# Optimization experiments

Hardware: AMD Instinct MI355X
Metric: run time of the kernel (lower is better)

## Reference

```python
import jax, jax.numpy as jnp
import numpy as np

B, IN, H = 4096, 1024, 2048


def setup_inputs() -> dict:
    key = jax.random.key(0)
    ks = jax.random.split(key, 7)
    return {
        "x": jax.random.normal(ks[0], (B, IN), jnp.float32),
        "h": jax.random.normal(ks[1], (B, H), jnp.float32),
        "c": jax.random.normal(ks[2], (B, H), jnp.float32),
        "w_ih": jax.random.normal(ks[3], (4 * H, IN), jnp.float32) * 0.02,
        "w_hh": jax.random.normal(ks[4], (4 * H, H), jnp.float32) * 0.02,
        "b_ih": jax.random.normal(ks[5], (4 * H,), jnp.float32) * 0.02,
        "b_hh": jax.random.normal(ks[6], (4 * H,), jnp.float32) * 0.02,
    }


def reference(x, h, c, w_ih, w_hh, b_ih, b_hh):
    act = jnp.sin  # custom gate activation (Sine_activation repo)
    # Combined GEMMs: same math as the 8 separate F.linear calls.
    # gates: [B, 4H], chunk order along dim 0 of weights: f, i, ic, o
    gates = (x @ w_ih.T + b_ih) + (h @ w_hh.T + b_hh)
    f_in, i_in, ic_in, o_in = jnp.split(gates, 4, axis=-1)
    ft = jax.nn.sigmoid(f_in)
    it = jax.nn.sigmoid(i_in)
    i_cands = act(ic_in)
    ct = c * ft + i_cands * it
    ot = jax.nn.sigmoid(o_in)
    ht = ot * act(ct)
    return (ht, ct)
```

## Files before the change

### kernel.cpp

```cpp
#include <hip/hip_runtime.h>

typedef __attribute__((ext_vector_type(8))) short short8;
typedef __attribute__((ext_vector_type(4))) float f32x4;

#define BDIM 4096
#define INDIM 1024
#define HDIM 2048
#define KDIM 3072
#define NDIM 8192
#define OUT_HALF 8388608
#define NKT 96

__device__ __forceinline__ unsigned short f2bf(float f) {
  unsigned u = __float_as_uint(f);
  u += 0x7FFFu + ((u >> 16) & 1u);
  return (unsigned short)(u >> 16);
}

__device__ __forceinline__ float sigmoidf_(float x) {
  return 1.0f / (1.0f + __expf(-x));
}

__global__ __launch_bounds__(256) void pack_a(const float* __restrict__ x,
                                              const float* __restrict__ hh,
                                              unsigned short* __restrict__ A) {
  int idx = blockIdx.x * 256 + threadIdx.x;
  int m = idx / 384;
  int k0 = (idx - m * 384) * 8;
  const float* src = (k0 < INDIM) ? (x + (size_t)m * INDIM + k0)
                                  : (hh + (size_t)m * HDIM + (k0 - INDIM));
  float4 lo = ((const float4*)src)[0];
  float4 hi = ((const float4*)src)[1];
  union { unsigned short us[8]; uint4 v; } o;
  o.us[0] = f2bf(lo.x); o.us[1] = f2bf(lo.y); o.us[2] = f2bf(lo.z); o.us[3] = f2bf(lo.w);
  o.us[4] = f2bf(hi.x); o.us[5] = f2bf(hi.y); o.us[6] = f2bf(hi.z); o.us[7] = f2bf(hi.w);
  *(uint4*)(A + (size_t)m * KDIM + k0) = o.v;
}

__global__ __launch_bounds__(256) void pack_w(const float* __restrict__ w_ih,
                                              const float* __restrict__ w_hh,
                                              const float* __restrict__ b_ih,
                                              const float* __restrict__ b_hh,
                                              unsigned short* __restrict__ W,
                                              float* __restrict__ bias) {
  int idx = blockIdx.x * 256 + threadIdx.x;
  int np = idx / 384;
  int rem = idx - np * 384;
  int k0 = rem * 8;
  int j = np >> 2;
  int g = np & 3;
  int n = g * HDIM + j;
  const float* src = (k0 < INDIM) ? (w_ih + (size_t)n * INDIM + k0)
                                  : (w_hh + (size_t)n * HDIM + (k0 - INDIM));
  float4 lo = ((const float4*)src)[0];
  float4 hi = ((const float4*)src)[1];
  union { unsigned short us[8]; uint4 v; } o;
  o.us[0] = f2bf(lo.x); o.us[1] = f2bf(lo.y); o.us[2] = f2bf(lo.z); o.us[3] = f2bf(lo.w);
  o.us[4] = f2bf(hi.x); o.us[5] = f2bf(hi.y); o.us[6] = f2bf(hi.z); o.us[7] = f2bf(hi.w);
  *(uint4*)(W + (size_t)np * KDIM + k0) = o.v;
  if (rem == 0) bias[np] = b_ih[n] + b_hh[n];
}

__device__ __forceinline__ void gload_lds16(const void* g, void* l) {
  __builtin_amdgcn_global_load_lds(
      (const __attribute__((address_space(1))) void*)g,
      (__attribute__((address_space(3))) void*)l, 16, 0, 0);
}

#define SB0 __builtin_amdgcn_sched_barrier(0)

__global__ __launch_bounds__(512, 2) void lstm_gemm(
    const unsigned short* __restrict__ A,
    const unsigned short* __restrict__ W,
    const float* __restrict__ bias,
    const float* __restrict__ c,
    float* __restrict__ out) {
  extern __shared__ char smem[];

  const int tid = threadIdx.x;
  const int lane = tid & 63;
  const int wid = tid >> 6;

  const int bid = blockIdx.x;
  const int local = bid >> 3;
  const int tm = (bid & 7) * 2 + (local & 1);
  const int tn = local >> 1;

  int rowA0, clA0, rowA1, clA1;
  {
    int P0 = wid * 1024 + lane * 16;
    int P1 = 8192 + wid * 1024 + lane * 16;
    int r2, cp, cg;
    r2 = P0 >> 7; cp = (P0 >> 4) & 7; cg = cp ^ (r2 & 7);
    rowA0 = r2 * 2 + (cg >> 2); clA0 = cg & 3;
    r2 = P1 >> 7; cp = (P1 >> 4) & 7; cg = cp ^ (r2 & 7);
    rowA1 = r2 * 2 + (cg >> 2); clA1 = cg & 3;
  }
  const unsigned short* srcA0 = A + (size_t)(tm * 256 + rowA0) * KDIM + clA0 * 8;
  const unsigned short* srcA1 = A + (size_t)(tm * 256 + rowA1) * KDIM + clA1 * 8;
  const unsigned short* srcB0 = W + (size_t)(tn * 256 + rowA0) * KDIM + clA0 * 8;
  const unsigned short* srcB1 = W + (size_t)(tn * 256 + rowA1) * KDIM + clA1 * 8;
  const int ldA0 = wid * 1024;
  const int ldA1 = 8192 + wid * 1024;
  const int ldB0 = 16384 + wid * 1024;
  const int ldB1 = 24576 + wid * 1024;

  const int fr = lane & 15;
  const int fq = lane >> 4;
  const int wr = wid >> 2;
  const int wc = wid & 3;
  const int frh = fr >> 1;
  const int clA = (((fr & 1) << 2) | fq) ^ frh;
  const int aconst = wr * 8192 + frh * 128 + clA * 16;
  const int bconst = 16384 + wc * 4096 + frh * 128 + clA * 16;

  f32x4 acc[8][4] = {};
  short8 af[4], bf_[4], ag[4];

#pragma unroll
  for (int tt = 0; tt < 3; ++tt) {
    char* lb = smem + tt * 32768;
    gload_lds16(srcA0 + tt * 32, lb + ldA0);
    gload_lds16(srcA1 + tt * 32, lb + ldA1);
    gload_lds16(srcB0 + tt * 32, lb + ldB0);
    gload_lds16(srcB1 + tt * 32, lb + ldB1);
  }
  asm volatile("s_waitcnt vmcnt(8)" ::: "memory");
  __builtin_amdgcn_s_barrier(); SB0;
#pragma unroll
  for (int mi = 0; mi < 4; ++mi)
    af[mi] = *(const short8*)(smem + aconst + mi * 1024);
#pragma unroll
  for (int ni = 0; ni < 4; ++ni)
    bf_[ni] = *(const short8*)(smem + bconst + ni * 1024);

#define TILE_BODY(T, VMSTR, STAGE_, PREF_)                                   \
  do {                                                                       \
    const char* rb = smem + ((T) & 3) * 32768;                               \
    const char* rbn = smem + (((T) + 1) & 3) * 32768;                        \
    char* lb = smem + (((T) + 3) & 3) * 32768;                               \
    if (STAGE_) {                                                            \
      gload_lds16(srcA0 + (size_t)((T) + 3) * 32, lb + ldA0);                \
      gload_lds16(srcA1 + (size_t)((T) + 3) * 32, lb + ldA1);                \
    }                                                                        \
    _Pragma("unroll")                                                        \
    for (int mi = 0; mi < 4; ++mi)                                           \
      ag[mi] = *(const short8*)(rb + aconst + (mi + 4) * 1024);              \
    SB0;                                                                     \
    __builtin_amdgcn_s_setprio(1);                                           \
    _Pragma("unroll")                                                        \
    for (int mi = 0; mi < 4; ++mi)                                           \
      _Pragma("unroll")                                                      \
      for (int ni = 0; ni < 4; ++ni)                                         \
        acc[mi][ni] = __builtin_amdgcn_mfma_f32_16x16x32_bf16(               \
            af[mi], bf_[ni], acc[mi][ni], 0, 0, 0);                          \
    __builtin_amdgcn_s_setprio(0);                                           \
    if (STAGE_) {                                                            \
      gload_lds16(srcB0 + (size_t)((T) + 3) * 32, lb + ldB0);                \
      gload_lds16(srcB1 + (size_t)((T) + 3) * 32, lb + ldB1);                \
    }                                                                        \
    asm volatile("s_waitcnt vmcnt(" VMSTR ")" ::: "memory");                 \
    asm volatile("s_waitcnt lgkmcnt(0)" ::: "memory");                       \
    __builtin_amdgcn_s_barrier(); SB0;                                       \
    if (PREF_) {                                                             \
      _Pragma("unroll")                                                      \
      for (int mi = 0; mi < 4; ++mi)                                         \
        af[mi] = *(const short8*)(rbn + aconst + mi * 1024);                 \
    }                                                                        \
    SB0;                                                                     \
    __builtin_amdgcn_s_setprio(1);                                           \
    _Pragma("unroll")                                                        \
    for (int mi = 0; mi < 4; ++mi)                                           \
      _Pragma("unroll")                                                      \
      for (int ni = 0; ni < 4; ++ni)                                         \
        acc[mi + 4][ni] = __builtin_amdgcn_mfma_f32_16x16x32_bf16(           \
            ag[mi], bf_[ni], acc[mi + 4][ni], 0, 0, 0);                      \
    __builtin_amdgcn_s_setprio(0);                                           \
    if (PREF_) {                                                             \
      _Pragma("unroll")                                                      \
      for (int ni = 0; ni < 4; ++ni)                                         \
        bf_[ni] = *(const short8*)(rbn + bconst + ni * 1024);                \
    }                                                                        \
  } while (0)

  for (int t = 0; t < NKT - 3; ++t) TILE_BODY(t, "8", true, true);
  TILE_BODY(NKT - 3, "4", false, true);
  TILE_BODY(NKT - 2, "0", false, true);
  TILE_BODY(NKT - 1, "0", false, false);
#undef TILE_BODY

  const int jw = fr;
  const int jg = tn * 64 + wc * 16 + jw;
  const f32x4 bi = *(const f32x4*)(bias + tn * 256 + wc * 64 + jw * 4);
  float* ep = (float*)smem + wid * 1024;

#pragma unroll
  for (int mi = 0; mi < 8; ++mi) {
#pragma unroll
    for (int ni = 0; ni < 4; ++ni)
#pragma unroll
      for (int r = 0; r < 4; ++r)
        ep[(fq * 4 + r) * 64 + ni * 16 + fr] = acc[mi][ni][r];
    asm volatile("s_waitcnt lgkmcnt(0)" ::: "memory");
#pragma unroll
    for (int t4 = 0; t4 < 4; ++t4) {
      const int row = fq + t4 * 4;
      f32x4 g4 = *(const f32x4*)(ep + row * 64 + jw * 4);
      const float f_in = g4[0] + bi[0];
      const float i_in = g4[1] + bi[1];
      const float ic_in = g4[2] + bi[2];
      const float o_in = g4[3] + bi[3];
      const float ft = sigmoidf_(f_in);
      const float it = sigmoidf_(i_in);
      const float ics = __sinf(ic_in);
      const int mg = tm * 256 + wr * 128 + mi * 16 + row;
      const float cv = c[(size_t)mg * HDIM + jg];
      const float ct = cv * ft + ics * it;
      const float ot = sigmoidf_(o_in);
      const float ht = ot * __sinf(ct);
      out[(size_t)mg * HDIM + jg] = ht;
      out[OUT_HALF + (size_t)mg * HDIM + jg] = ct;
    }
    asm volatile("s_waitcnt lgkmcnt(0)" ::: "memory");
  }
}

extern "C" void kernel_launch(void* const* d_in, const int* in_sizes, int n_in,
                              void* d_out, int out_size, void* d_ws, size_t ws_size,
                              hipStream_t stream) {
  const float* x    = (const float*)d_in[0];
  const float* h    = (const float*)d_in[1];
  const float* c    = (const float*)d_in[2];
  const float* w_ih = (const float*)d_in[3];
  const float* w_hh = (const float*)d_in[4];
  const float* b_ih = (const float*)d_in[5];
  const float* b_hh = (const float*)d_in[6];
  float* out = (float*)d_out;

  char* ws = (char*)d_ws;
  unsigned short* Abf = (unsigned short*)ws;
  unsigned short* Wbf = (unsigned short*)(ws + 25165824);
  float* bias = (float*)(ws + 25165824 + 50331648);

  hipFuncSetAttribute((const void*)lstm_gemm,
                      hipFuncAttributeMaxDynamicSharedMemorySize, 131072);

  pack_a<<<6144, 256, 0, stream>>>(x, h, Abf);
  pack_w<<<12288, 256, 0, stream>>>(w_ih, w_hh, b_ih, b_hh, Wbf, bias);
  lstm_gemm<<<512, 512, 131072, stream>>>(Abf, Wbf, bias, c, out);
}
```

Before: 222.6 us.

## Shrink GEMM block tile to 128x256 with 4 waves and triple-buffered LDS

New measurement: 258.3 us. 1.16x slower.

```diff
diff --git a/kernel.cpp b/kernel.cpp
--- a/kernel.cpp
+++ b/kernel.cpp
@@ -10,6 +10,7 @@
 #define NDIM 8192
 #define OUT_HALF 8388608
 #define NKT 96
+#define BUFB 24576
 
 __device__ __forceinline__ unsigned short f2bf(float f) {
   unsigned u = __float_as_uint(f);
@@ -69,7 +70,7 @@
 
 #define SB0 __builtin_amdgcn_sched_barrier(0)
 
-__global__ __launch_bounds__(512, 2) void lstm_gemm(
+__global__ __launch_bounds__(256, 2) void lstm_gemm(
     const unsigned short* __restrict__ A,
     const unsigned short* __restrict__ W,
     const float* __restrict__ bias,
@@ -83,69 +84,74 @@
 
   const int bid = blockIdx.x;
   const int local = bid >> 3;
-  const int tm = (bid & 7) * 2 + (local & 1);
-  const int tn = local >> 1;
-
-  int rowA0, clA0, rowA1, clA1;
-  {
-    int P0 = wid * 1024 + lane * 16;
-    int P1 = 8192 + wid * 1024 + lane * 16;
-    int r2, cp, cg;
-    r2 = P0 >> 7; cp = (P0 >> 4) & 7; cg = cp ^ (r2 & 7);
-    rowA0 = r2 * 2 + (cg >> 2); clA0 = cg & 3;
-    r2 = P1 >> 7; cp = (P1 >> 4) & 7; cg = cp ^ (r2 & 7);
-    rowA1 = r2 * 2 + (cg >> 2); clA1 = cg & 3;
+  const int tn = (bid & 7) * 4 + (local >> 5);
+  const int tm = local & 31;
+
+  int rowQ[4], colQ[4];
+#pragma unroll
+  for (int q = 0; q < 4; ++q) {
+    int P = q * 4096 + wid * 1024 + lane * 16;
+    int r2 = P >> 7, cp = (P >> 4) & 7, cg = cp ^ (r2 & 7);
+    rowQ[q] = r2 * 2 + (cg >> 2);
+    colQ[q] = (cg & 3) * 8;
   }
-  const unsigned short* srcA0 = A + (size_t)(tm * 256 + rowA0) * KDIM + clA0 * 8;
-  const unsigned short* srcA1 = A + (size_t)(tm * 256 + rowA1) * KDIM + clA1 * 8;
-  const unsigned short* srcB0 = W + (size_t)(tn * 256 + rowA0) * KDIM + clA0 * 8;
-  const unsigned short* srcB1 = W + (size_t)(tn * 256 + rowA1) * KDIM + clA1 * 8;
-  const int ldA0 = wid * 1024;
-  const int ldA1 = 8192 + wid * 1024;
-  const int ldB0 = 16384 + wid * 1024;
-  const int ldB1 = 24576 + wid * 1024;
+  const unsigned short* sA0 = A + (size_t)(tm * 128 + rowQ[0]) * KDIM + colQ[0];
+  const unsigned short* sA1 = A + (size_t)(tm * 128 + rowQ[1]) * KDIM + colQ[1];
+  const unsigned short* sB0 = W + (size_t)(tn * 256 + rowQ[0]) * KDIM + colQ[0];
+  const unsigned short* sB1 = W + (size_t)(tn * 256 + rowQ[1]) * KDIM + colQ[1];
+  const unsigned short* sB2 = W + (size_t)(tn * 256 + rowQ[2]) * KDIM + colQ[2];
+  const unsigned short* sB3 = W + (size_t)(tn * 256 + rowQ[3]) * KDIM + colQ[3];
+  const int dA0 = wid * 1024;
+  const int dA1 = 4096 + wid * 1024;
+  const int dB0 = 8192 + wid * 1024;
+  const int dB1 = 12288 + wid * 1024;
+  const int dB2 = 16384 + wid * 1024;
+  const int dB3 = 20480 + wid * 1024;
 
   const int fr = lane & 15;
   const int fq = lane >> 4;
-  const int wr = wid >> 2;
-  const int wc = wid & 3;
   const int frh = fr >> 1;
   const int clA = (((fr & 1) << 2) | fq) ^ frh;
-  const int aconst = wr * 8192 + frh * 128 + clA * 16;
-  const int bconst = 16384 + wc * 4096 + frh * 128 + clA * 16;
+  const int aconst = frh * 128 + clA * 16;
+  const int bconst = 8192 + wid * 4096 + frh * 128 + clA * 16;
 
   f32x4 acc[8][4] = {};
   short8 af[4], bf_[4], ag[4];
 
-#pragma unroll
-  for (int tt = 0; tt < 3; ++tt) {
-    char* lb = smem + tt * 32768;
-    gload_lds16(srcA0 + tt * 32, lb + ldA0);
-    gload_lds16(srcA1 + tt * 32, lb + ldA1);
-    gload_lds16(srcB0 + tt * 32, lb + ldB0);
-    gload_lds16(srcB1 + tt * 32, lb + ldB1);
-  }
-  asm volatile("s_waitcnt vmcnt(8)" ::: "memory");
+  char* b0 = smem;
+  char* b1 = smem + BUFB;
+  char* b2 = smem + 2 * BUFB;
+
+#define STAGE_TILE(K, LB)                                   \
+  do {                                                      \
+    gload_lds16(sA0 + (size_t)(K) * 32, (LB) + dA0);        \
+    gload_lds16(sA1 + (size_t)(K) * 32, (LB) + dA1);        \
+    gload_lds16(sB0 + (size_t)(K) * 32, (LB) + dB0);        \
+    gload_lds16(sB1 + (size_t)(K) * 32, (LB) + dB1);        \
+    gload_lds16(sB2 + (size_t)(K) * 32, (LB) + dB2);        \
+    gload_lds16(sB3 + (size_t)(K) * 32, (LB) + dB3);        \
+  } while (0)
+
+  STAGE_TILE(0, b0);
+  STAGE_TILE(1, b1);
+  asm volatile("s_waitcnt vmcnt(6)" ::: "memory");
   __builtin_amdgcn_s_barrier(); SB0;
 #pragma unroll
   for (int mi = 0; mi < 4; ++mi)
-    af[mi] = *(const short8*)(smem + aconst + mi * 1024);
+    af[mi] = *(const short8*)(b0 + aconst + mi * 1024);
 #pragma unroll
   for (int ni = 0; ni < 4; ++ni)
-    bf_[ni] = *(const short8*)(smem + bconst + ni * 1024);
-
-#define TILE_BODY(T, VMSTR, STAGE_, PREF_)                                   \
+    bf_[ni] = *(const short8*)(b0 + bconst + ni * 1024);
+
+#define BODY(T, RB, RBN, LB, VMSTR, STG, STAGE_, PREF_)                      \
   do {                                                                       \
-    const char* rb = smem + ((T) & 3) * 32768;                               \
-    const char* rbn = smem + (((T) + 1) & 3) * 32768;                        \
-    char* lb = smem + (((T) + 3) & 3) * 32768;                               \
     if (STAGE_) {                                                            \
-      gload_lds16(srcA0 + (size_t)((T) + 3) * 32, lb + ldA0);                \
-      gload_lds16(srcA1 + (size_t)((T) + 3) * 32, lb + ldA1);                \
+      gload_lds16(sA0 + (size_t)(STG) * 32, (LB) + dA0);                     \
+      gload_lds16(sA1 + (size_t)(STG) * 32, (LB) + dA1);                     \
     }                                                                        \
     _Pragma("unroll")                                                        \
     for (int mi = 0; mi < 4; ++mi)                                           \
-      ag[mi] = *(const short8*)(rb + aconst + (mi + 4) * 1024);              \
+      ag[mi] = *(const short8*)((RB) + aconst + (mi + 4) * 1024);            \
     SB0;                                                                     \
     __builtin_amdgcn_s_setprio(1);                                           \
     _Pragma("unroll")                                                        \
@@ -156,8 +162,10 @@
             af[mi], bf_[ni], acc[mi][ni], 0, 0, 0);                          \
     __builtin_amdgcn_s_setprio(0);                                           \
     if (STAGE_) {                                                            \
-      gload_lds16(srcB0 + (size_t)((T) + 3) * 32, lb + ldB0);                \
-      gload_lds16(srcB1 + (size_t)((T) + 3) * 32, lb + ldB1);                \
+      gload_lds16(sB0 + (size_t)(STG) * 32, (LB) + dB0);                     \
+      gload_lds16(sB1 + (size_t)(STG) * 32, (LB) + dB1);                     \
+      gload_lds16(sB2 + (size_t)(STG) * 32, (LB) + dB2);                     \
+      gload_lds16(sB3 + (size_t)(STG) * 32, (LB) + dB3);                     \
     }                                                                        \
     asm volatile("s_waitcnt vmcnt(" VMSTR ")" ::: "memory");                 \
     asm volatile("s_waitcnt lgkmcnt(0)" ::: "memory");                       \
@@ -165,7 +173,7 @@
     if (PREF_) {                                                             \
       _Pragma("unroll")                                                      \
       for (int mi = 0; mi < 4; ++mi)                                         \
-        af[mi] = *(const short8*)(rbn + aconst + mi * 1024);                 \
+        af[mi] = *(const short8*)((RBN) + aconst + mi * 1024);               \
     }                                                                        \
     SB0;                                                                     \
     __builtin_amdgcn_s_setprio(1);                                           \
@@ -179,20 +187,25 @@
     if (PREF_) {                                                             \
       _Pragma("unroll")                                                      \
       for (int ni = 0; ni < 4; ++ni)                                         \
-        bf_[ni] = *(const short8*)(rbn + bconst + ni * 1024);                \
+        bf_[ni] = *(const short8*)((RBN) + bconst + ni * 1024);              \
     }                                                                        \
   } while (0)
 
-  for (int t = 0; t < NKT - 3; ++t) TILE_BODY(t, "8", true, true);
-  TILE_BODY(NKT - 3, "4", false, true);
-  TILE_BODY(NKT - 2, "0", false, true);
-  TILE_BODY(NKT - 1, "0", false, false);
-#undef TILE_BODY
+  for (int t = 0; t < NKT - 3; t += 3) {
+    BODY(t,     b0, b1, b2, "6", t + 2, true, true);
+    BODY(t + 1, b1, b2, b0, "6", t + 3, true, true);
+    BODY(t + 2, b2, b0, b1, "6", t + 4, true, true);
+  }
+  BODY(NKT - 3, b0, b1, b2, "6", NKT - 1, true, true);
+  BODY(NKT - 2, b1, b2, b0, "0", 0, false, true);
+  BODY(NKT - 1, b2, b0, b1, "0", 0, false, false);
+#undef BODY
+#undef STAGE_TILE
 
   const int jw = fr;
-  const int jg = tn * 64 + wc * 16 + jw;
-  const f32x4 bi = *(const f32x4*)(bias + tn * 256 + wc * 64 + jw * 4);
-  float* ep = (float*)smem + wid * 1024;
+  const int jg = tn * 64 + wid * 16 + jw;
+  const f32x4 bi = *(const f32x4*)(bias + tn * 256 + wid * 64 + jw * 4);
+  float* ep = (float*)(smem) + wid * 1152;
 
 #pragma unroll
   for (int mi = 0; mi < 8; ++mi) {
@@ -200,12 +213,12 @@
     for (int ni = 0; ni < 4; ++ni)
 #pragma unroll
       for (int r = 0; r < 4; ++r)
-        ep[(fq * 4 + r) * 64 + ni * 16 + fr] = acc[mi][ni][r];
+        ep[(fq * 4 + r) * 68 + ni * 16 + fr] = acc[mi][ni][r];
     asm volatile("s_waitcnt lgkmcnt(0)" ::: "memory");
 #pragma unroll
     for (int t4 = 0; t4 < 4; ++t4) {
       const int row = fq + t4 * 4;
-      f32x4 g4 = *(const f32x4*)(ep + row * 64 + jw * 4);
+      f32x4 g4 = *(const f32x4*)(ep + row * 68 + jw * 4);
       const float f_in = g4[0] + bi[0];
       const float i_in = g4[1] + bi[1];
       const float ic_in = g4[2] + bi[2];
@@ -213,7 +226,7 @@
       const float ft = sigmoidf_(f_in);
       const float it = sigmoidf_(i_in);
       const float ics = __sinf(ic_in);
-      const int mg = tm * 256 + wr * 128 + mi * 16 + row;
+      const int mg = tm * 128 + mi * 16 + row;
       const float cv = c[(size_t)mg * HDIM + jg];
       const float ct = cv * ft + ics * it;
       const float ot = sigmoidf_(o_in);
@@ -243,9 +256,9 @@
   float* bias = (float*)(ws + 25165824 + 50331648);
 
   hipFuncSetAttribute((const void*)lstm_gemm,
-                      hipFuncAttributeMaxDynamicSharedMemorySize, 131072);
+                      hipFuncAttributeMaxDynamicSharedMemorySize, 73728);
 
   pack_a<<<6144, 256, 0, stream>>>(x, h, Abf);
   pack_w<<<12288, 256, 0, stream>>>(w_ih, w_hh, b_ih, b_hh, Wbf, bias);
-  lstm_gemm<<<512, 512, 131072, stream>>>(Abf, Wbf, bias, c, out);
-}
+  lstm_gemm<<<1024, 256, 73728, stream>>>(Abf, Wbf, bias, c, out);
+}
```

## Switch GEMM to 32x32x16 MFMA tiles and merge pack kernels

Applied to the files above, without the earlier changes.

New measurement: 235.1 us. +5.6%, slower.

```diff
diff --git a/kernel.cpp b/kernel.cpp
--- a/kernel.cpp
+++ b/kernel.cpp
@@ -2,6 +2,7 @@
 
 typedef __attribute__((ext_vector_type(8))) short short8;
 typedef __attribute__((ext_vector_type(4))) float f32x4;
+typedef __attribute__((ext_vector_type(16))) float f32x16;
 
 #define BDIM 4096
 #define INDIM 1024
@@ -10,6 +11,7 @@
 #define NDIM 8192
 #define OUT_HALF 8388608
 #define NKT 96
+#define ACHUNKS 1572864
 
 __device__ __forceinline__ unsigned short f2bf(float f) {
   unsigned u = __float_as_uint(f);
@@ -21,44 +23,42 @@
   return 1.0f / (1.0f + __expf(-x));
 }
 
-__global__ __launch_bounds__(256) void pack_a(const float* __restrict__ x,
-                                              const float* __restrict__ hh,
-                                              unsigned short* __restrict__ A) {
+__global__ __launch_bounds__(256) void pack_all(
+    const float* __restrict__ x, const float* __restrict__ hh,
+    const float* __restrict__ w_ih, const float* __restrict__ w_hh,
+    const float* __restrict__ b_ih, const float* __restrict__ b_hh,
+    unsigned short* __restrict__ A, unsigned short* __restrict__ W,
+    float* __restrict__ bias) {
   int idx = blockIdx.x * 256 + threadIdx.x;
-  int m = idx / 384;
-  int k0 = (idx - m * 384) * 8;
-  const float* src = (k0 < INDIM) ? (x + (size_t)m * INDIM + k0)
-                                  : (hh + (size_t)m * HDIM + (k0 - INDIM));
-  float4 lo = ((const float4*)src)[0];
-  float4 hi = ((const float4*)src)[1];
-  union { unsigned short us[8]; uint4 v; } o;
-  o.us[0] = f2bf(lo.x); o.us[1] = f2bf(lo.y); o.us[2] = f2bf(lo.z); o.us[3] = f2bf(lo.w);
-  o.us[4] = f2bf(hi.x); o.us[5] = f2bf(hi.y); o.us[6] = f2bf(hi.z); o.us[7] = f2bf(hi.w);
-  *(uint4*)(A + (size_t)m * KDIM + k0) = o.v;
-}
-
-__global__ __launch_bounds__(256) void pack_w(const float* __restrict__ w_ih,
-                                              const float* __restrict__ w_hh,
-                                              const float* __restrict__ b_ih,
-                                              const float* __restrict__ b_hh,
-                                              unsigned short* __restrict__ W,
-                                              float* __restrict__ bias) {
-  int idx = blockIdx.x * 256 + threadIdx.x;
-  int np = idx / 384;
-  int rem = idx - np * 384;
-  int k0 = rem * 8;
-  int j = np >> 2;
-  int g = np & 3;
-  int n = g * HDIM + j;
-  const float* src = (k0 < INDIM) ? (w_ih + (size_t)n * INDIM + k0)
-                                  : (w_hh + (size_t)n * HDIM + (k0 - INDIM));
-  float4 lo = ((const float4*)src)[0];
-  float4 hi = ((const float4*)src)[1];
-  union { unsigned short us[8]; uint4 v; } o;
-  o.us[0] = f2bf(lo.x); o.us[1] = f2bf(lo.y); o.us[2] = f2bf(lo.z); o.us[3] = f2bf(lo.w);
-  o.us[4] = f2bf(hi.x); o.us[5] = f2bf(hi.y); o.us[6] = f2bf(hi.z); o.us[7] = f2bf(hi.w);
-  *(uint4*)(W + (size_t)np * KDIM + k0) = o.v;
-  if (rem == 0) bias[np] = b_ih[n] + b_hh[n];
+  if (idx < ACHUNKS) {
+    int m = idx / 384;
+    int k0 = (idx - m * 384) * 8;
+    const float* src = (k0 < INDIM) ? (x + (size_t)m * INDIM + k0)
+                                    : (hh + (size_t)m * HDIM + (k0 - INDIM));
+    float4 lo = ((const float4*)src)[0];
+    float4 hi = ((const float4*)src)[1];
+    union { unsigned short us[8]; uint4 v; } o;
+    o.us[0] = f2bf(lo.x); o.us[1] = f2bf(lo.y); o.us[2] = f2bf(lo.z); o.us[3] = f2bf(lo.w);
+    o.us[4] = f2bf(hi.x); o.us[5] = f2bf(hi.y); o.us[6] = f2bf(hi.z); o.us[7] = f2bf(hi.w);
+    *(uint4*)(A + (size_t)m * KDIM + k0) = o.v;
+  } else {
+    idx -= ACHUNKS;
+    int np = idx / 384;
+    int rem = idx - np * 384;
+    int k0 = rem * 8;
+    int j = np >> 2;
+    int g = np & 3;
+    int n = g * HDIM + j;
+    const float* src = (k0 < INDIM) ? (w_ih + (size_t)n * INDIM + k0)
+                                    : (w_hh + (size_t)n * HDIM + (k0 - INDIM));
+    float4 lo = ((const float4*)src)[0];
+    float4 hi = ((const float4*)src)[1];
+    union { unsigned short us[8]; uint4 v; } o;
+    o.us[0] = f2bf(lo.x); o.us[1] = f2bf(lo.y); o.us[2] = f2bf(lo.z); o.us[3] = f2bf(lo.w);
+    o.us[4] = f2bf(hi.x); o.us[5] = f2bf(hi.y); o.us[6] = f2bf(hi.z); o.us[7] = f2bf(hi.w);
+    *(uint4*)(W + (size_t)np * KDIM + k0) = o.v;
+    if (rem == 0) bias[np] = b_ih[n] + b_hh[n];
+  }
 }
 
 __device__ __forceinline__ void gload_lds16(const void* g, void* l) {
@@ -96,43 +96,50 @@
     r2 = P1 >> 7; cp = (P1 >> 4) & 7; cg = cp ^ (r2 & 7);
     rowA1 = r2 * 2 + (cg >> 2); clA1 = cg & 3;
   }
-  const unsigned short* srcA0 = A + (size_t)(tm * 256 + rowA0) * KDIM + clA0 * 8;
-  const unsigned short* srcA1 = A + (size_t)(tm * 256 + rowA1) * KDIM + clA1 * 8;
-  const unsigned short* srcB0 = W + (size_t)(tn * 256 + rowA0) * KDIM + clA0 * 8;
-  const unsigned short* srcB1 = W + (size_t)(tn * 256 + rowA1) * KDIM + clA1 * 8;
+  const unsigned short* gA0 = A + (size_t)(tm * 256 + rowA0) * KDIM + clA0 * 8;
+  const unsigned short* gA1 = A + (size_t)(tm * 256 + rowA1) * KDIM + clA1 * 8;
+  const unsigned short* gB0 = W + (size_t)(tn * 256 + rowA0) * KDIM + clA0 * 8;
+  const unsigned short* gB1 = W + (size_t)(tn * 256 + rowA1) * KDIM + clA1 * 8;
   const int ldA0 = wid * 1024;
   const int ldA1 = 8192 + wid * 1024;
   const int ldB0 = 16384 + wid * 1024;
   const int ldB1 = 24576 + wid * 1024;
 
-  const int fr = lane & 15;
-  const int fq = lane >> 4;
+  const int r5 = lane & 31;
+  const int kb = lane >> 5;
   const int wr = wid >> 2;
   const int wc = wid & 3;
-  const int frh = fr >> 1;
-  const int clA = (((fr & 1) << 2) | fq) ^ frh;
-  const int aconst = wr * 8192 + frh * 128 + clA * 16;
-  const int bconst = 16384 + wc * 4096 + frh * 128 + clA * 16;
-
-  f32x4 acc[8][4] = {};
-  short8 af[4], bf_[4], ag[4];
+  int aoff[2];
+#pragma unroll
+  for (int kh = 0; kh < 2; ++kh) {
+    int cp = (((r5 & 1) << 2) + kh * 2 + kb) ^ ((r5 >> 1) & 7);
+    aoff[kh] = (r5 >> 1) * 128 + cp * 16;
+  }
+  const int abase = wr * 8192;
+  const int bbase = 16384 + wc * 4096;
+
+  f32x16 acc[4][2] = {};
+  short8 af[4], ag[4], bf_[2][2];
 
 #pragma unroll
   for (int tt = 0; tt < 3; ++tt) {
     char* lb = smem + tt * 32768;
-    gload_lds16(srcA0 + tt * 32, lb + ldA0);
-    gload_lds16(srcA1 + tt * 32, lb + ldA1);
-    gload_lds16(srcB0 + tt * 32, lb + ldB0);
-    gload_lds16(srcB1 + tt * 32, lb + ldB1);
+    gload_lds16(gA0, lb + ldA0);
+    gload_lds16(gA1, lb + ldA1);
+    gload_lds16(gB0, lb + ldB0);
+    gload_lds16(gB1, lb + ldB1);
+    gA0 += 32; gA1 += 32; gB0 += 32; gB1 += 32;
   }
   asm volatile("s_waitcnt vmcnt(8)" ::: "memory");
   __builtin_amdgcn_s_barrier(); SB0;
 #pragma unroll
-  for (int mi = 0; mi < 4; ++mi)
-    af[mi] = *(const short8*)(smem + aconst + mi * 1024);
-#pragma unroll
-  for (int ni = 0; ni < 4; ++ni)
-    bf_[ni] = *(const short8*)(smem + bconst + ni * 1024);
+  for (int mt = 0; mt < 4; ++mt)
+    af[mt] = *(const short8*)(smem + abase + mt * 2048 + aoff[0]);
+#pragma unroll
+  for (int nt = 0; nt < 2; ++nt)
+#pragma unroll
+    for (int kh = 0; kh < 2; ++kh)
+      bf_[nt][kh] = *(const short8*)(smem + bbase + nt * 2048 + aoff[kh]);
 
 #define TILE_BODY(T, VMSTR, STAGE_, PREF_)                                   \
   do {                                                                       \
@@ -140,46 +147,49 @@
     const char* rbn = smem + (((T) + 1) & 3) * 32768;                        \
     char* lb = smem + (((T) + 3) & 3) * 32768;                               \
     if (STAGE_) {                                                            \
-      gload_lds16(srcA0 + (size_t)((T) + 3) * 32, lb + ldA0);                \
-      gload_lds16(srcA1 + (size_t)((T) + 3) * 32, lb + ldA1);                \
+      gload_lds16(gA0, lb + ldA0);                                           \
+      gload_lds16(gA1, lb + ldA1);                                           \
     }                                                                        \
     _Pragma("unroll")                                                        \
-    for (int mi = 0; mi < 4; ++mi)                                           \
-      ag[mi] = *(const short8*)(rb + aconst + (mi + 4) * 1024);              \
+    for (int mt = 0; mt < 4; ++mt)                                           \
+      ag[mt] = *(const short8*)(rb + abase + mt * 2048 + aoff[1]);           \
     SB0;                                                                     \
     __builtin_amdgcn_s_setprio(1);                                           \
     _Pragma("unroll")                                                        \
-    for (int mi = 0; mi < 4; ++mi)                                           \
-      _Pragma("unroll")                                                      \
-      for (int ni = 0; ni < 4; ++ni)                                         \
-        acc[mi][ni] = __builtin_amdgcn_mfma_f32_16x16x32_bf16(               \
-            af[mi], bf_[ni], acc[mi][ni], 0, 0, 0);                          \
+    for (int mt = 0; mt < 4; ++mt)                                           \
+      _Pragma("unroll")                                                      \
+      for (int nt = 0; nt < 2; ++nt)                                         \
+        acc[mt][nt] = __builtin_amdgcn_mfma_f32_32x32x16_bf16(               \
+            af[mt], bf_[nt][0], acc[mt][nt], 0, 0, 0);                       \
     __builtin_amdgcn_s_setprio(0);                                           \
     if (STAGE_) {                                                            \
-      gload_lds16(srcB0 + (size_t)((T) + 3) * 32, lb + ldB0);                \
-      gload_lds16(srcB1 + (size_t)((T) + 3) * 32, lb + ldB1);                \
+      gload_lds16(gB0, lb + ldB0);                                           \
+      gload_lds16(gB1, lb + ldB1);                                           \
+      gA0 += 32; gA1 += 32; gB0 += 32; gB1 += 32;                            \
     }                                                                        \
     asm volatile("s_waitcnt vmcnt(" VMSTR ")" ::: "memory");                 \
     asm volatile("s_waitcnt lgkmcnt(0)" ::: "memory");                       \
     __builtin_amdgcn_s_barrier(); SB0;                                       \
     if (PREF_) {                                                             \
       _Pragma("unroll")                                                      \
-      for (int mi = 0; mi < 4; ++mi)                                         \
-        af[mi] = *(const short8*)(rbn + aconst + mi * 1024);                 \
+      for (int mt = 0; mt < 4; ++mt)                                         \
+        af[mt] = *(const short8*)(rbn + abase + mt * 2048 + aoff[0]);        \
     }                                                                        \
     SB0;                                                                     \
     __builtin_amdgcn_s_setprio(1);                                           \
     _Pragma("unroll")                                                        \
-    for (int mi = 0; mi < 4; ++mi)                                           \
-      _Pragma("unroll")                                                      \
-      for (int ni = 0; ni < 4; ++ni)                                         \
-        acc[mi + 4][ni] = __builtin_amdgcn_mfma_f32_16x16x32_bf16(           \
-            ag[mi], bf_[ni], acc[mi + 4][ni], 0, 0, 0);                      \
+    for (int mt = 0; mt < 4; ++mt)                                           \
+      _Pragma("unroll")                                                      \
+      for (int nt = 0; nt < 2; ++nt)                                         \
+        acc[mt][nt] = __builtin_amdgcn_mfma_f32_32x32x16_bf16(               \
+            ag[mt], bf_[nt][1], acc[mt][nt], 0, 0, 0);                       \
     __builtin_amdgcn_s_setprio(0);                                           \
     if (PREF_) {                                                             \
       _Pragma("unroll")                                                      \
-      for (int ni = 0; ni < 4; ++ni)                                         \
-        bf_[ni] = *(const short8*)(rbn + bconst + ni * 1024);                \
+      for (int nt = 0; nt < 2; ++nt)                                         \
+        _Pragma("unroll")                                                    \
+        for (int kh = 0; kh < 2; ++kh)                                       \
+          bf_[nt][kh] = *(const short8*)(rbn + bbase + nt * 2048 + aoff[kh]);\
     }                                                                        \
   } while (0)
 
@@ -189,23 +199,23 @@
   TILE_BODY(NKT - 1, "0", false, false);
 #undef TILE_BODY
 
-  const int jw = fr;
-  const int jg = tn * 64 + wc * 16 + jw;
-  const f32x4 bi = *(const f32x4*)(bias + tn * 256 + wc * 64 + jw * 4);
-  float* ep = (float*)smem + wid * 1024;
-
-#pragma unroll
-  for (int mi = 0; mi < 8; ++mi) {
-#pragma unroll
-    for (int ni = 0; ni < 4; ++ni)
-#pragma unroll
-      for (int r = 0; r < 4; ++r)
-        ep[(fq * 4 + r) * 64 + ni * 16 + fr] = acc[mi][ni][r];
+  const int jr = lane & 15;
+  const int rowg = lane >> 4;
+  const f32x4 bi = *(const f32x4*)(bias + tn * 256 + wc * 64 + jr * 4);
+  float* ep = (float*)smem + wid * 2176;
+
+#pragma unroll
+  for (int mt = 0; mt < 4; ++mt) {
+#pragma unroll
+    for (int nt = 0; nt < 2; ++nt)
+#pragma unroll
+      for (int r = 0; r < 16; ++r)
+        ep[((r & 3) + 8 * (r >> 2) + 4 * kb) * 68 + nt * 32 + r5] = acc[mt][nt][r];
     asm volatile("s_waitcnt lgkmcnt(0)" ::: "memory");
 #pragma unroll
-    for (int t4 = 0; t4 < 4; ++t4) {
-      const int row = fq + t4 * 4;
-      f32x4 g4 = *(const f32x4*)(ep + row * 64 + jw * 4);
+    for (int t4 = 0; t4 < 8; ++t4) {
+      const int row = rowg + t4 * 4;
+      f32x4 g4 = *(const f32x4*)(ep + row * 68 + jr * 4);
       const float f_in = g4[0] + bi[0];
       const float i_in = g4[1] + bi[1];
       const float ic_in = g4[2] + bi[2];
@@ -213,7 +223,8 @@
       const float ft = sigmoidf_(f_in);
       const float it = sigmoidf_(i_in);
       const float ics = __sinf(ic_in);
-      const int mg = tm * 256 + wr * 128 + mi * 16 + row;
+      const int mg = tm * 256 + wr * 128 + mt * 32 + row;
+      const int jg = tn * 64 + wc * 16 + jr;
       const float cv = c[(size_t)mg * HDIM + jg];
       const float ct = cv * ft + ics * it;
       const float ot = sigmoidf_(o_in);
@@ -245,7 +256,6 @@
   hipFuncSetAttribute((const void*)lstm_gemm,
                       hipFuncAttributeMaxDynamicSharedMemorySize, 131072);
 
-  pack_a<<<6144, 256, 0, stream>>>(x, h, Abf);
-  pack_w<<<12288, 256, 0, stream>>>(w_ih, w_hh, b_ih, b_hh, Wbf, bias);
+  pack_all<<<18432, 256, 0, stream>>>(x, h, w_ih, w_hh, b_ih, b_hh, Abf, Wbf, bias);
   lstm_gemm<<<512, 512, 131072, stream>>>(Abf, Wbf, bias, c, out);
 }
```
